# Kernel optimization log

Measured on AMD Instinct MI355X. Metric: run time of the kernel, lower is better.

The kernel has to match this reference:

```python
import jax, jax.numpy as jnp
import numpy as np

DIM = 192
D_STATE = 16
D_CONV = 4
EXPAND = 2
D_INNER = EXPAND * DIM
DT_RANK = -(-DIM // 16)  # ceil(dim/16) = 12


def setup_inputs() -> dict:
    key = jax.random.key(0)
    ks = jax.random.split(key, 10)
    b, c, h, w = 4, DIM, 64, 64
    s = 0.02
    return {
        "x": jax.random.normal(ks[0], (b, c, h, w), dtype=jnp.float32),
        "in_proj_w": jax.random.normal(ks[1], (2 * D_INNER, DIM), dtype=jnp.float32) * s,
        "conv_w": jax.random.normal(ks[2], (D_INNER, D_CONV), dtype=jnp.float32) * s,
        "conv_b": jax.random.normal(ks[3], (D_INNER,), dtype=jnp.float32) * s,
        "x_proj_w": jax.random.normal(ks[4], (DT_RANK + 2 * D_STATE, D_INNER), dtype=jnp.float32) * s,
        "dt_proj_w": jax.random.normal(ks[5], (D_INNER, DT_RANK), dtype=jnp.float32) * s,
        "dt_proj_b": jax.random.normal(ks[6], (D_INNER,), dtype=jnp.float32) * 0.5 - 4.0,
        "A_log": jnp.log(jnp.broadcast_to(jnp.arange(1, D_STATE + 1, dtype=jnp.float32), (D_INNER, D_STATE))),
        "D_param": jnp.ones((D_INNER,), dtype=jnp.float32),
        "out_proj_w": jax.random.normal(ks[7], (DIM, D_INNER), dtype=jnp.float32) * s,
    }


def _mamba(xs, in_proj_w, conv_w, conv_b, x_proj_w, dt_proj_w, dt_proj_b, A_log, D_param, out_proj_w):
    # xs: [b, L, dim]
    b, L, _ = xs.shape
    xz = jnp.einsum("bld,ed->ble", xs, in_proj_w)            # [b, L, 2*D_INNER]
    xp, z = jnp.split(xz, 2, axis=-1)                          # each [b, L, D_INNER]

    # causal depthwise conv1d over L
    xt = jnp.transpose(xp, (0, 2, 1))                          # [b, D_INNER, L]
    k = conv_w[:, None, :]                                     # [D_INNER, 1, K]
    xc = jax.lax.conv_general_dilated(
        xt, k, window_strides=(1,), padding=[(D_CONV - 1, 0)],
        feature_group_count=D_INNER,
        dimension_numbers=("NCH", "OIH", "NCH"))
    xc = xc + conv_b[None, :, None]
    xc = jax.nn.silu(jnp.transpose(xc, (0, 2, 1)))             # [b, L, D_INNER]

    x_dbl = jnp.einsum("bld,ed->ble", xc, x_proj_w)           # [b, L, DT_RANK+2N]
    dt_r = x_dbl[..., :DT_RANK]
    Bmat = x_dbl[..., DT_RANK:DT_RANK + D_STATE]               # [b, L, N]
    Cmat = x_dbl[..., DT_RANK + D_STATE:]                      # [b, L, N]

    dt = jax.nn.softplus(jnp.einsum("blr,dr->bld", dt_r, dt_proj_w) + dt_proj_b)  # [b, L, D_INNER]
    A = -jnp.exp(A_log)                                        # [D_INNER, N]

    deltaA = jnp.exp(dt[..., None] * A[None, None])            # [b, L, D, N]
    deltaBx = dt[..., None] * Bmat[:, :, None, :] * xc[..., None]  # [b, L, D, N]

    def combine(e1, e2):
        a1, b1 = e1
        a2, b2 = e2
        return a1 * a2, a2 * b1 + b2

    _, hstates = jax.lax.associative_scan(combine, (deltaA, deltaBx), axis=1)
    y = jnp.einsum("bldn,bln->bld", hstates, Cmat) + D_param * xc
    y = y * jax.nn.silu(z)
    return jnp.einsum("bld,ed->ble", y, out_proj_w)            # [b, L, dim]


def reference(x, in_proj_w, conv_w, conv_b, x_proj_w, dt_proj_w, dt_proj_b, A_log, D_param, out_proj_w):
    b, c, h, w = x.shape
    xs = jnp.transpose(x.reshape(b, c, h * w), (0, 2, 1))      # [b, L, c]
    y = _mamba(xs, in_proj_w, conv_w, conv_b, x_proj_w, dt_proj_w, dt_proj_b, A_log, D_param, out_proj_w)
    return jnp.transpose(y, (0, 2, 1)).reshape(b, c, h, w)
```

## Files before the change

### kernel.cpp

```cpp
#include <hip/hip_runtime.h>
#include <math.h>

#define BN   4
#define CD   192
#define LSEQ 4096
#define DI   384
#define DTRK 12
#define DS   16
#define NJ   44
#define KC   (CD / 8)
#define TILE_U (KC * 16 * 8)
#define KC2  (DI / 8)
#define TILE2_U (KC2 * 16 * 8)

typedef __attribute__((ext_vector_type(8))) short  short8;
typedef __attribute__((ext_vector_type(8))) unsigned short ushort8;
typedef __attribute__((ext_vector_type(4))) float  float4v;

__device__ __forceinline__ float silu_f(float x) { return x / (1.f + __expf(-x)); }
__device__ __forceinline__ float softplus_f(float x) {
    return (x > 15.f) ? x : log1pf(__expf(x));
}
__device__ __forceinline__ unsigned short bf16_rn(float v) {
    unsigned int u = __float_as_uint(v);
    unsigned int r = (u + 0x7FFFu + ((u >> 16) & 1u)) >> 16;
    return (unsigned short)r;
}
__device__ __forceinline__ float bf16_to_f(unsigned short h) {
    return __uint_as_float(((unsigned int)h) << 16);
}
#define BDEC(V0, V1, i) bf16_to_f(((i) < 8) ? (V0)[(i)] : (V1)[(i) - 8])

template<int CTRL, int RM>
__device__ __forceinline__ float dpp_prev(float x, float ident) {
    return __uint_as_float((unsigned)__builtin_amdgcn_update_dpp(
        (int)__float_as_uint(ident), (int)__float_as_uint(x), CTRL, RM, 0xF, false));
}

template<int CTRL, int RM>
__device__ __forceinline__ void scan_step2(float& Pa, float& Ha, float& Pb, float& Hb) {
    float Ppa = dpp_prev<CTRL, RM>(Pa, 1.0f);
    float Hpa = dpp_prev<CTRL, RM>(Ha, 0.0f);
    float Ppb = dpp_prev<CTRL, RM>(Pb, 1.0f);
    float Hpb = dpp_prev<CTRL, RM>(Hb, 0.0f);
    Ha = fmaf(Pa, Hpa, Ha);  Pa *= Ppa;
    Hb = fmaf(Pb, Hpb, Hb);  Pb *= Ppb;
}

__device__ __forceinline__ void wave_scan_ph2(float& Pa, float& Ha,
                                              float& Pb, float& Hb) {
    scan_step2<0x111, 0xF>(Pa, Ha, Pb, Hb);
    scan_step2<0x112, 0xF>(Pa, Ha, Pb, Hb);
    scan_step2<0x114, 0xF>(Pa, Ha, Pb, Hb);
    scan_step2<0x118, 0xF>(Pa, Ha, Pb, Hb);
    scan_step2<0x142, 0xA>(Pa, Ha, Pb, Hb);
    scan_step2<0x143, 0xC>(Pa, Ha, Pb, Hb);
}

__global__ __launch_bounds__(256) void k_wsplit(const float* __restrict__ w,
                                                unsigned short* __restrict__ whi,
                                                unsigned short* __restrict__ wlo) {
    const int t = blockIdx.x * 256 + threadIdx.x;
    const int e = t / KC, kc = t % KC;
    const float* src = w + (size_t)e * CD + kc * 8;
    unsigned short uh[8], ul[8];
#pragma unroll
    for (int j = 0; j < 8; ++j) {
        float v = src[j];
        unsigned short h = bf16_rn(v);
        uh[j] = h;
        ul[j] = bf16_rn(v - bf16_to_f(h));
    }
    const size_t dst = ((size_t)(e >> 4) * KC + kc) * 128 + (size_t)(e & 15) * 8;
    *(ushort8*)(whi + dst) = (ushort8){uh[0],uh[1],uh[2],uh[3],uh[4],uh[5],uh[6],uh[7]};
    *(ushort8*)(wlo + dst) = (ushort8){ul[0],ul[1],ul[2],ul[3],ul[4],ul[5],ul[6],ul[7]};
}

__global__ __launch_bounds__(256) void k_xsplit(const float* __restrict__ x,
                                                unsigned short* __restrict__ xhi,
                                                unsigned short* __restrict__ xlo) {
    __shared__ float sx[CD * 65];
    const int b = blockIdx.y;
    const int lt0 = blockIdx.x * 64;
    const int wave = threadIdx.x >> 6, lane = threadIdx.x & 63;
#pragma unroll 4
    for (int pass = 0; pass < 48; ++pass) {
        int c = pass * 4 + wave;
        sx[c * 65 + lane] = x[((size_t)b * CD + c) * LSEQ + lt0 + lane];
    }
    __syncthreads();
    const int l = threadIdx.x >> 2, cq = threadIdx.x & 3;
    const size_t tbase = ((size_t)b * 256 + (lt0 >> 4) + (l >> 4)) * TILE_U + (size_t)(l & 15) * 8;
#pragma unroll
    for (int m = 0; m < 6; ++m) {
        const int kc = cq * 6 + m;
        unsigned short uh[8], ul[8];
#pragma unroll
        for (int j = 0; j < 8; ++j) {
            float v = sx[(kc * 8 + j) * 65 + l];
            unsigned short h = bf16_rn(v);
            uh[j] = h;
            ul[j] = bf16_rn(v - bf16_to_f(h));
        }
        const size_t dst = tbase + (size_t)kc * 128;
        *(ushort8*)(xhi + dst) = (ushort8){uh[0],uh[1],uh[2],uh[3],uh[4],uh[5],uh[6],uh[7]};
        *(ushort8*)(xlo + dst) = (ushort8){ul[0],ul[1],ul[2],ul[3],ul[4],ul[5],ul[6],ul[7]};
    }
}

__global__ __launch_bounds__(256, 4) void k_inproj_mfma(const unsigned short* __restrict__ xhi,
                                                        const unsigned short* __restrict__ xlo,
                                                        const unsigned short* __restrict__ whi,
                                                        const unsigned short* __restrict__ wlo,
                                                        float* __restrict__ xp,
                                                        float* __restrict__ zs) {
    const int b = blockIdx.z;
    const int e0 = blockIdx.y * 32;
    const int wave = threadIdx.x >> 6, lane = threadIdx.x & 63;
    const int l0 = blockIdx.x * 256 + wave * 64;
    const int n16 = lane & 15, quad = lane >> 4;
    const size_t laneoff = (size_t)quad * 128 + (size_t)n16 * 8;

    const unsigned short* xb_h[4];
    const unsigned short* xb_l[4];
#pragma unroll
    for (int ln = 0; ln < 4; ++ln) {
        const int lt = (l0 >> 4) + ln;
        size_t off = ((size_t)b * 256 + lt) * TILE_U + laneoff;
        xb_h[ln] = xhi + off;
        xb_l[ln] = xlo + off;
    }
    const unsigned short* wb_h[2];
    const unsigned short* wb_l[2];
#pragma unroll
    for (int em = 0; em < 2; ++em) {
        const int et = (e0 >> 4) + em;
        size_t off = (size_t)et * TILE_U + laneoff;
        wb_h[em] = whi + off;
        wb_l[em] = wlo + off;
    }

    float4v acc[2][4];
#pragma unroll
    for (int em = 0; em < 2; ++em)
#pragma unroll
        for (int ln = 0; ln < 4; ++ln) acc[em][ln] = (float4v){0.f, 0.f, 0.f, 0.f};

#pragma unroll
    for (int kk = 0; kk < CD; kk += 32) {
        const size_t ko = (size_t)kk * 16;
        short8 bh[4], bl[4], ah[2], al[2];
#pragma unroll
        for (int ln = 0; ln < 4; ++ln) {
            bh[ln] = *(const short8*)(xb_h[ln] + ko);
            bl[ln] = *(const short8*)(xb_l[ln] + ko);
        }
#pragma unroll
        for (int em = 0; em < 2; ++em) {
            ah[em] = *(const short8*)(wb_h[em] + ko);
            al[em] = *(const short8*)(wb_l[em] + ko);
        }
#pragma unroll
        for (int em = 0; em < 2; ++em)
#pragma unroll
            for (int ln = 0; ln < 4; ++ln) {
                acc[em][ln] = __builtin_amdgcn_mfma_f32_16x16x32_bf16(ah[em], bh[ln], acc[em][ln], 0, 0, 0);
                acc[em][ln] = __builtin_amdgcn_mfma_f32_16x16x32_bf16(ah[em], bl[ln], acc[em][ln], 0, 0, 0);
                acc[em][ln] = __builtin_amdgcn_mfma_f32_16x16x32_bf16(al[em], bh[ln], acc[em][ln], 0, 0, 0);
            }
    }
    const bool is_z = (e0 >= DI);
#pragma unroll
    for (int em = 0; em < 2; ++em) {
#pragma unroll
        for (int r = 0; r < 4; ++r) {
            int row = e0 + em * 16 + quad * 4 + r;
            if (is_z) row -= DI;
            float* dst = (is_z ? zs : xp) + ((size_t)b * DI + row) * LSEQ;
#pragma unroll
            for (int ln = 0; ln < 4; ++ln) {
                float v = acc[em][ln][r];
                if (is_z) v = silu_f(v);
                dst[l0 + ln * 16 + n16] = v;
            }
        }
    }
}

__global__ __launch_bounds__(256) void k_conv(const float* __restrict__ xp,
                                              const float* __restrict__ cw,
                                              const float* __restrict__ cb,
                                              float* __restrict__ xc) {
    const int d = blockIdx.y, b = blockIdx.z;
    const int l0 = blockIdx.x * 1024 + threadIdx.x * 4;
    const float w0 = cw[d * 4 + 0], w1 = cw[d * 4 + 1], w2 = cw[d * 4 + 2], w3 = cw[d * 4 + 3];
    const float bb = cb[d];
    const float* row = xp + ((size_t)b * DI + d) * LSEQ;
    float4 cur = *(const float4*)(row + l0);
    float4 pv;
    if (l0 == 0) pv = make_float4(0.f, 0.f, 0.f, 0.f);
    else         pv = *(const float4*)(row + l0 - 4);
    float o0 = fmaf(w0, pv.y, fmaf(w1, pv.z, fmaf(w2, pv.w, fmaf(w3, cur.x, bb))));
    float o1 = fmaf(w0, pv.z, fmaf(w1, pv.w, fmaf(w2, cur.x, fmaf(w3, cur.y, bb))));
    float o2 = fmaf(w0, pv.w, fmaf(w1, cur.x, fmaf(w2, cur.y, fmaf(w3, cur.z, bb))));
    float o3 = fmaf(w0, cur.x, fmaf(w1, cur.y, fmaf(w2, cur.z, fmaf(w3, cur.w, bb))));
    float4 o = make_float4(silu_f(o0), silu_f(o1), silu_f(o2), silu_f(o3));
    *(float4*)(xc + ((size_t)b * DI + d) * LSEQ + l0) = o;
}

__global__ __launch_bounds__(256) void k_xdbl(const float* __restrict__ xc,
                                              const float* __restrict__ xpw,
                                              float* __restrict__ xdp) {
    const int part = blockIdx.y & 3, jg = blockIdx.y >> 2, b = blockIdx.z;
    const int l = blockIdx.x * 256 + threadIdx.x;
    const int d0 = part * 96;
    const int j0 = jg * 11;
    float acc[11];
#pragma unroll
    for (int j = 0; j < 11; ++j) acc[j] = 0.f;
    const float* xcb = xc + ((size_t)b * DI + d0) * LSEQ + l;
    const float* wb  = xpw + (size_t)j0 * DI + d0;
    for (int dd = 0; dd < 96; dd += 4) {
        float v0 = xcb[(size_t)dd * LSEQ];
        float v1 = xcb[(size_t)(dd + 1) * LSEQ];
        float v2 = xcb[(size_t)(dd + 2) * LSEQ];
        float v3 = xcb[(size_t)(dd + 3) * LSEQ];
#pragma unroll
        for (int j = 0; j < 11; ++j) {
            const float* wj = wb + (size_t)j * DI + dd;
            acc[j] = fmaf(wj[0], v0, fmaf(wj[1], v1, fmaf(wj[2], v2, fmaf(wj[3], v3, acc[j]))));
        }
    }
    float* dst = xdp + (size_t)(part * BN + b) * NJ * LSEQ + (size_t)j0 * LSEQ + l;
#pragma unroll
    for (int j = 0; j < 11; ++j) dst[(size_t)j * LSEQ] = acc[j];
}

__global__ __launch_bounds__(256) void k_xdbl_reduce(const float* __restrict__ xdp,
                                                     float* __restrict__ dtr,
                                                     unsigned short* __restrict__ Bm,
                                                     unsigned short* __restrict__ Cm) {
    const int j = blockIdx.y, b = blockIdx.z;
    const int l = blockIdx.x * 256 + threadIdx.x;
    float s = 0.f;
#pragma unroll
    for (int p = 0; p < 4; ++p)
        s += xdp[(size_t)(p * BN + b) * NJ * LSEQ + (size_t)j * LSEQ + l];
    if (j < DTRK)            dtr[((size_t)b * DTRK + j) * LSEQ + l] = s;
    else if (j < DTRK + DS)  Bm[((size_t)b * DS + (j - DTRK)) * LSEQ + l] = bf16_rn(s);
    else                     Cm[((size_t)b * DS + (j - DTRK - DS)) * LSEQ + l] = bf16_rn(s);
}

__global__ __launch_bounds__(256) void k_dt(const float* __restrict__ dtr,
                                            const float* __restrict__ dtw,
                                            const float* __restrict__ dtb,
                                            float* __restrict__ dt) {
    const int e0 = blockIdx.y * 16, b = blockIdx.z;
    const int l = blockIdx.x * 256 + threadIdx.x;
    float acc[16];
#pragma unroll
    for (int e = 0; e < 16; ++e) acc[e] = 0.f;
    const float* rb = dtr + (size_t)b * DTRK * LSEQ + l;
#pragma unroll
    for (int r = 0; r < DTRK; ++r) {
        float v = rb[(size_t)r * LSEQ];
#pragma unroll
        for (int e = 0; e < 16; ++e)
            acc[e] = fmaf(dtw[(size_t)(e0 + e) * DTRK + r], v, acc[e]);
    }
    float* dst = dt + ((size_t)b * DI + e0) * LSEQ + l;
#pragma unroll
    for (int e = 0; e < 16; ++e) dst[(size_t)e * LSEQ] = softplus_f(acc[e] + dtb[e0 + e]);
}

__global__ __launch_bounds__(256) void k_scan(const float* __restrict__ dtb,
                                              const float* __restrict__ xc,
                                              const unsigned short* __restrict__ Bm,
                                              const unsigned short* __restrict__ Cm,
                                              const float* __restrict__ zs,
                                              const float* __restrict__ A_log,
                                              const float* __restrict__ Dp,
                                              float* __restrict__ g) {
    __shared__ float sP[DS][4];
    __shared__ float sH[DS][4];
    const int d = blockIdx.x, b = blockIdx.y;
    const int t = threadIdx.x;
    const int wave = t >> 6, lane = t & 63;
    const size_t rowoff = ((size_t)b * DI + d) * LSEQ;
    const int l0 = t * 16;

    const unsigned short* Bp = Bm + (size_t)b * DS * LSEQ + l0;
    const unsigned short* Cp = Cm + (size_t)b * DS * LSEQ + l0;

    float dt16[16], dx16[16];
#pragma unroll
    for (int i = 0; i < 16; i += 4) {
        float4 dv = *(const float4*)(dtb + rowoff + l0 + i);
        float4 xv = *(const float4*)(xc + rowoff + l0 + i);
        dt16[i+0] = dv.x; dt16[i+1] = dv.y; dt16[i+2] = dv.z; dt16[i+3] = dv.w;
        dx16[i+0] = dv.x * xv.x; dx16[i+1] = dv.y * xv.y;
        dx16[i+2] = dv.z * xv.z; dx16[i+3] = dv.w * xv.w;
    }
    const float* Alogd = A_log + (size_t)d * DS;
    float y16[16];
#pragma unroll
    for (int i = 0; i < 16; ++i) y16[i] = 0.f;

#pragma unroll 1
    for (int np = 0; np < 8; ++np) {
        const int n = 2 * np;
        const float Ana = -__expf(Alogd[n]);
        const float Anb = -__expf(Alogd[n + 1]);
        float PCa[16], PCb[16];
#pragma unroll
        for (int i = 0; i < 16; ++i) {
            PCa[i] = __expf(dt16[i] * Ana);
            PCb[i] = __expf(dt16[i] * Anb);
        }

        const size_t nla = (size_t)n * LSEQ;
        const size_t nlb = (size_t)(n + 1) * LSEQ;
        ushort8 Bu0 = *(const ushort8*)(Bp + nla);
        ushort8 Bu1 = *(const ushort8*)(Bp + nla + 8);
        ushort8 Bv0 = *(const ushort8*)(Bp + nlb);
        ushort8 Bv1 = *(const ushort8*)(Bp + nlb + 8);
        ushort8 Cu0 = *(const ushort8*)(Cp + nla);
        ushort8 Cu1 = *(const ushort8*)(Cp + nla + 8);
        ushort8 Cv0 = *(const ushort8*)(Cp + nlb);
        ushort8 Cv1 = *(const ushort8*)(Cp + nlb + 8);

        float ha = 0.f, hb = 0.f, pa = 1.f, pb = 1.f;
#pragma unroll
        for (int i = 0; i < 16; ++i) {
            float Bai = BDEC(Bu0, Bu1, i), Bbi = BDEC(Bv0, Bv1, i);
            float Cai = BDEC(Cu0, Cu1, i), Cbi = BDEC(Cv0, Cv1, i);
            ha = fmaf(PCa[i], ha, dx16[i] * Bai);
            pa *= PCa[i];
            y16[i] = fmaf(ha, Cai, y16[i]);
            PCa[i] = pa * Cai;
            hb = fmaf(PCb[i], hb, dx16[i] * Bbi);
            pb *= PCb[i];
            y16[i] = fmaf(hb, Cbi, y16[i]);
            PCb[i] = pb * Cbi;
        }

        wave_scan_ph2(pa, ha, pb, hb);
        if (lane == 63) {
            sP[n][wave] = pa;     sH[n][wave] = ha;
            sP[n+1][wave] = pb;   sH[n+1][wave] = hb;
        }
        float Pea = __shfl_up(pa, 1u), Hea = __shfl_up(ha, 1u);
        float Peb = __shfl_up(pb, 1u), Heb = __shfl_up(hb, 1u);
        if (lane == 0) { Pea = 1.f; Hea = 0.f; Peb = 1.f; Heb = 0.f; }
        __syncthreads();
        float hca = 0.f, hcb = 0.f;
#pragma unroll
        for (int ww = 0; ww < 3; ++ww)
            if (ww < wave) {
                hca = fmaf(sP[n][ww], hca, sH[n][ww]);
                hcb = fmaf(sP[n+1][ww], hcb, sH[n+1][ww]);
            }
        float hva = fmaf(Pea, hca, Hea);
        float hvb = fmaf(Peb, hcb, Heb);
#pragma unroll
        for (int i = 0; i < 16; ++i) {
            y16[i] = fmaf(hva, PCa[i], y16[i]);
            y16[i] = fmaf(hvb, PCb[i], y16[i]);
        }
    }
    const float Dd = Dp[d];
#pragma unroll
    for (int i = 0; i < 16; i += 4) {
        float4 xv = *(const float4*)(xc + rowoff + l0 + i);
        float4 zv = *(const float4*)(zs + rowoff + l0 + i);
        float4 o;
        o.x = fmaf(Dd, xv.x, y16[i+0]) * zv.x;
        o.y = fmaf(Dd, xv.y, y16[i+1]) * zv.y;
        o.z = fmaf(Dd, xv.z, y16[i+2]) * zv.z;
        o.w = fmaf(Dd, xv.w, y16[i+3]) * zv.w;
        *(float4*)(g + rowoff + l0 + i) = o;
    }
}

__global__ __launch_bounds__(256) void k_gsplit(const float* __restrict__ g,
                                                unsigned short* __restrict__ ghi,
                                                unsigned short* __restrict__ glo) {
    __shared__ float sx[DI * 33];
    const int b = blockIdx.y;
    const int lt0 = blockIdx.x * 32;
#pragma unroll 4
    for (int i = threadIdx.x; i < DI * 32; i += 256) {
        int row = i >> 5, l = i & 31;
        sx[row * 33 + l] = g[((size_t)b * DI + row) * LSEQ + lt0 + l];
    }
    __syncthreads();
    const int l = threadIdx.x >> 3, oct = threadIdx.x & 7;
    const int lt = blockIdx.x * 2 + (l >> 4);
    const size_t tbase = ((size_t)b * 256 + lt) * TILE2_U + (size_t)(l & 15) * 8;
#pragma unroll
    for (int m = 0; m < 6; ++m) {
        const int kc = oct * 6 + m;
        unsigned short uh[8], ul[8];
#pragma unroll
        for (int j = 0; j < 8; ++j) {
            float v = sx[(kc * 8 + j) * 33 + l];
            unsigned short h = bf16_rn(v);
            uh[j] = h;
            ul[j] = bf16_rn(v - bf16_to_f(h));
        }
        const size_t dst = tbase + (size_t)kc * 128;
        *(ushort8*)(ghi + dst) = (ushort8){uh[0],uh[1],uh[2],uh[3],uh[4],uh[5],uh[6],uh[7]};
        *(ushort8*)(glo + dst) = (ushort8){ul[0],ul[1],ul[2],ul[3],ul[4],ul[5],ul[6],ul[7]};
    }
}

__global__ __launch_bounds__(256) void k_woutsplit(const float* __restrict__ w,
                                                   unsigned short* __restrict__ whi,
                                                   unsigned short* __restrict__ wlo) {
    const int t = blockIdx.x * 256 + threadIdx.x;
    const int e = t / KC2, kc = t % KC2;
    const float* src = w + (size_t)e * DI + kc * 8;
    unsigned short uh[8], ul[8];
#pragma unroll
    for (int j = 0; j < 8; ++j) {
        float v = src[j];
        unsigned short h = bf16_rn(v);
        uh[j] = h;
        ul[j] = bf16_rn(v - bf16_to_f(h));
    }
    const size_t dst = ((size_t)(e >> 4) * KC2 + kc) * 128 + (size_t)(e & 15) * 8;
    *(ushort8*)(whi + dst) = (ushort8){uh[0],uh[1],uh[2],uh[3],uh[4],uh[5],uh[6],uh[7]};
    *(ushort8*)(wlo + dst) = (ushort8){ul[0],ul[1],ul[2],ul[3],ul[4],ul[5],ul[6],ul[7]};
}

__global__ __launch_bounds__(256, 4) void k_outproj_mfma(const unsigned short* __restrict__ ghi,
                                                         const unsigned short* __restrict__ glo,
                                                         const unsigned short* __restrict__ whi,
                                                         const unsigned short* __restrict__ wlo,
                                                         float* __restrict__ out) {
    const int b = blockIdx.z;
    const int c0 = blockIdx.y * 32;
    const int wave = threadIdx.x >> 6, lane = threadIdx.x & 63;
    const int l0 = blockIdx.x * 128 + wave * 32;
    const int n16 = lane & 15, quad = lane >> 4;
    const size_t laneoff = (size_t)quad * 128 + (size_t)n16 * 8;

    const unsigned short* gb_h[2];
    const unsigned short* gb_l[2];
#pragma unroll
    for (int ln = 0; ln < 2; ++ln) {
        const int lt = (l0 >> 4) + ln;
        size_t off = ((size_t)b * 256 + lt) * TILE2_U + laneoff;
        gb_h[ln] = ghi + off;
        gb_l[ln] = glo + off;
    }
    const unsigned short* wb_h[2];
    const unsigned short* wb_l[2];
#pragma unroll
    for (int em = 0; em < 2; ++em) {
        const int et = (c0 >> 4) + em;
        size_t off = (size_t)et * TILE2_U + laneoff;
        wb_h[em] = whi + off;
        wb_l[em] = wlo + off;
    }

    float4v acc[2][2];
#pragma unroll
    for (int em = 0; em < 2; ++em)
#pragma unroll
        for (int ln = 0; ln < 2; ++ln) acc[em][ln] = (float4v){0.f, 0.f, 0.f, 0.f};

#pragma unroll
    for (int kk = 0; kk < DI; kk += 32) {
        const size_t ko = (size_t)kk * 16;
        short8 bh[2], bl[2], ah[2], al[2];
#pragma unroll
        for (int ln = 0; ln < 2; ++ln) {
            bh[ln] = *(const short8*)(gb_h[ln] + ko);
            bl[ln] = *(const short8*)(gb_l[ln] + ko);
        }
#pragma unroll
        for (int em = 0; em < 2; ++em) {
            ah[em] = *(const short8*)(wb_h[em] + ko);
            al[em] = *(const short8*)(wb_l[em] + ko);
        }
#pragma unroll
        for (int em = 0; em < 2; ++em)
#pragma unroll
            for (int ln = 0; ln < 2; ++ln) {
                acc[em][ln] = __builtin_amdgcn_mfma_f32_16x16x32_bf16(ah[em], bh[ln], acc[em][ln], 0, 0, 0);
                acc[em][ln] = __builtin_amdgcn_mfma_f32_16x16x32_bf16(ah[em], bl[ln], acc[em][ln], 0, 0, 0);
                acc[em][ln] = __builtin_amdgcn_mfma_f32_16x16x32_bf16(al[em], bh[ln], acc[em][ln], 0, 0, 0);
            }
    }
#pragma unroll
    for (int em = 0; em < 2; ++em) {
#pragma unroll
        for (int r = 0; r < 4; ++r) {
            const int row = c0 + em * 16 + quad * 4 + r;
            float* dst = out + ((size_t)b * CD + row) * LSEQ;
#pragma unroll
            for (int ln = 0; ln < 2; ++ln)
                dst[l0 + ln * 16 + n16] = acc[em][ln][r];
        }
    }
}

extern "C" void kernel_launch(void* const* d_in, const int* in_sizes, int n_in,
                              void* d_out, int out_size, void* d_ws, size_t ws_size,
                              hipStream_t stream) {
    const float* x     = (const float*)d_in[0];
    const float* w_in  = (const float*)d_in[1];
    const float* cw    = (const float*)d_in[2];
    const float* cb    = (const float*)d_in[3];
    const float* xpw   = (const float*)d_in[4];
    const float* dtw   = (const float*)d_in[5];
    const float* dtbv  = (const float*)d_in[6];
    const float* A_log = (const float*)d_in[7];
    const float* Dp    = (const float*)d_in[8];
    const float* wout  = (const float*)d_in[9];
    float* out = (float*)d_out;

    float* ws = (float*)d_ws;
    const size_t NBL = (size_t)BN * DI * LSEQ;
    float* xp  = ws;
    float* zs  = xp + NBL;
    float* xc  = zs + NBL;
    float* dt  = xc + NBL;
    float* BmF = dt + NBL;
    unsigned short* Bm = (unsigned short*)BmF;
    unsigned short* Cm = Bm + (size_t)BN * LSEQ * DS;
    float* dtr = BmF + (size_t)BN * LSEQ * DS;
    float* xdp = dtr + (size_t)BN * DTRK * LSEQ;
    float* g   = xp;
    unsigned short* xhi = (unsigned short*)(xdp + 1048576);
    unsigned short* xlo = xhi + (size_t)BN * LSEQ * CD;
    unsigned short* whi = xlo + (size_t)BN * LSEQ * CD;
    unsigned short* wlo = whi + (size_t)(2 * DI) * CD;
    unsigned short* ghi  = (unsigned short*)zs;
    unsigned short* glo  = ghi + NBL;
    unsigned short* wohi = (unsigned short*)dtr;
    unsigned short* wolo = wohi + (size_t)CD * DI;

    k_wsplit      <<<dim3(72), 256, 0, stream>>>(w_in, whi, wlo);
    k_xsplit      <<<dim3(64, BN), 256, 0, stream>>>(x, xhi, xlo);
    k_inproj_mfma <<<dim3(16, 24, BN), 256, 0, stream>>>(xhi, xlo, whi, wlo, xp, zs);
    k_conv        <<<dim3(4, DI, BN), 256, 0, stream>>>(xp, cw, cb, xc);
    k_xdbl        <<<dim3(16, 16, BN), 256, 0, stream>>>(xc, xpw, xdp);
    k_xdbl_reduce <<<dim3(16, NJ, BN), 256, 0, stream>>>(xdp, dtr, Bm, Cm);
    k_dt          <<<dim3(16, 24, BN), 256, 0, stream>>>(dtr, dtw, dtbv, dt);
    k_scan        <<<dim3(DI, BN), 256, 0, stream>>>(dt, xc, Bm, Cm, zs, A_log, Dp, g);
    k_gsplit      <<<dim3(128, BN), 256, 0, stream>>>(g, ghi, glo);
    k_woutsplit   <<<dim3(36), 256, 0, stream>>>(wout, wohi, wolo);
    k_outproj_mfma<<<dim3(32, 6, BN), 256, 0, stream>>>(ghi, glo, wohi, wolo, out);
}
```

Measured before the change: 242.2 us.

## Split scan state dimension across two thread groups per block

The selective-scan kernel now launches 512 threads per block, with two groups of four waves each handling half of the 16 state channels over the full sequence. Partial outputs from the second group are passed through a 16 KB shared buffer and added by the first group before the epilogue. The aim is to double parallelism and shorten the serial per-thread loop over state channels. In exchange, each block loads dt and xc twice, needs extra shared memory and a block-wide barrier, and may fit fewer blocks per CU.

```diff
diff --git a/kernel.cpp b/kernel.cpp
--- a/kernel.cpp
+++ b/kernel.cpp
@@ -273,7 +273,7 @@
     for (int e = 0; e < 16; ++e) dst[(size_t)e * LSEQ] = softplus_f(acc[e] + dtb[e0 + e]);
 }
 
-__global__ __launch_bounds__(256) void k_scan(const float* __restrict__ dtb,
+__global__ __launch_bounds__(512) void k_scan(const float* __restrict__ dtb,
                                               const float* __restrict__ xc,
                                               const unsigned short* __restrict__ Bm,
                                               const unsigned short* __restrict__ Cm,
@@ -283,11 +283,14 @@
                                               float* __restrict__ g) {
     __shared__ float sP[DS][4];
     __shared__ float sH[DS][4];
+    __shared__ float sy[LSEQ];
     const int d = blockIdx.x, b = blockIdx.y;
     const int t = threadIdx.x;
-    const int wave = t >> 6, lane = t & 63;
+    const int w = t >> 6, lane = t & 63;
+    const int grp = w >> 2, wg = w & 3;
+    const int tl = t & 255;
     const size_t rowoff = ((size_t)b * DI + d) * LSEQ;
-    const int l0 = t * 16;
+    const int l0 = tl * 16;
 
     const unsigned short* Bp = Bm + (size_t)b * DS * LSEQ + l0;
     const unsigned short* Cp = Cm + (size_t)b * DS * LSEQ + l0;
@@ -306,9 +309,10 @@
 #pragma unroll
     for (int i = 0; i < 16; ++i) y16[i] = 0.f;
 
+    const int nbase = grp * 8;
 #pragma unroll 1
-    for (int np = 0; np < 8; ++np) {
-        const int n = 2 * np;
+    for (int np = 0; np < 4; ++np) {
+        const int n = nbase + 2 * np;
         const float Ana = -__expf(Alogd[n]);
         const float Anb = -__expf(Alogd[n + 1]);
         float PCa[16], PCb[16];
@@ -346,8 +350,8 @@
 
         wave_scan_ph2(pa, ha, pb, hb);
         if (lane == 63) {
-            sP[n][wave] = pa;     sH[n][wave] = ha;
-            sP[n+1][wave] = pb;   sH[n+1][wave] = hb;
+            sP[n][wg] = pa;     sH[n][wg] = ha;
+            sP[n+1][wg] = pb;   sH[n+1][wg] = hb;
         }
         float Pea = __shfl_up(pa, 1u), Hea = __shfl_up(ha, 1u);
         float Peb = __shfl_up(pb, 1u), Heb = __shfl_up(hb, 1u);
@@ -356,7 +360,7 @@
         float hca = 0.f, hcb = 0.f;
 #pragma unroll
         for (int ww = 0; ww < 3; ++ww)
-            if (ww < wave) {
+            if (ww < wg) {
                 hca = fmaf(sP[n][ww], hca, sH[n][ww]);
                 hcb = fmaf(sP[n+1][ww], hcb, sH[n+1][ww]);
             }
@@ -368,17 +372,27 @@
             y16[i] = fmaf(hvb, PCb[i], y16[i]);
         }
     }
-    const float Dd = Dp[d];
-#pragma unroll
-    for (int i = 0; i < 16; i += 4) {
-        float4 xv = *(const float4*)(xc + rowoff + l0 + i);
-        float4 zv = *(const float4*)(zs + rowoff + l0 + i);
-        float4 o;
-        o.x = fmaf(Dd, xv.x, y16[i+0]) * zv.x;
-        o.y = fmaf(Dd, xv.y, y16[i+1]) * zv.y;
-        o.z = fmaf(Dd, xv.z, y16[i+2]) * zv.z;
-        o.w = fmaf(Dd, xv.w, y16[i+3]) * zv.w;
-        *(float4*)(g + rowoff + l0 + i) = o;
+
+    if (grp == 1) {
+#pragma unroll
+        for (int i = 0; i < 16; i += 4)
+            *(float4*)(sy + l0 + i) = make_float4(y16[i], y16[i+1], y16[i+2], y16[i+3]);
+    }
+    __syncthreads();
+    if (grp == 0) {
+        const float Dd = Dp[d];
+#pragma unroll
+        for (int i = 0; i < 16; i += 4) {
+            float4 yp = *(const float4*)(sy + l0 + i);
+            float4 xv = *(const float4*)(xc + rowoff + l0 + i);
+            float4 zv = *(const float4*)(zs + rowoff + l0 + i);
+            float4 o;
+            o.x = fmaf(Dd, xv.x, y16[i+0] + yp.x) * zv.x;
+            o.y = fmaf(Dd, xv.y, y16[i+1] + yp.y) * zv.y;
+            o.z = fmaf(Dd, xv.z, y16[i+2] + yp.z) * zv.z;
+            o.w = fmaf(Dd, xv.w, y16[i+3] + yp.w) * zv.w;
+            *(float4*)(g + rowoff + l0 + i) = o;
+        }
     }
 }
 
@@ -549,7 +563,7 @@
     k_xdbl        <<<dim3(16, 16, BN), 256, 0, stream>>>(xc, xpw, xdp);
     k_xdbl_reduce <<<dim3(16, NJ, BN), 256, 0, stream>>>(xdp, dtr, Bm, Cm);
     k_dt          <<<dim3(16, 24, BN), 256, 0, stream>>>(dtr, dtw, dtbv, dt);
-    k_scan        <<<dim3(DI, BN), 256, 0, stream>>>(dt, xc, Bm, Cm, zs, A_log, Dp, g);
+    k_scan        <<<dim3(DI, BN), 512, 0, stream>>>(dt, xc, Bm, Cm, zs, A_log, Dp, g);
     k_gsplit      <<<dim3(128, BN), 256, 0, stream>>>(g, ghi, glo);
     k_woutsplit   <<<dim3(36), 256, 0, stream>>>(wout, wohi, wolo);
     k_outproj_mfma<<<dim3(32, 6, BN), 256, 0, stream>>>(ghi, glo, wohi, wolo, out);
```

Measured after the change: 257.1 us. 6.2% more time.
